# Performance work log

Measured on AMD Instinct MI355X. Metric: run time of the kernel, lower is better.

## Reference

```python
import math
import jax, jax.numpy as jnp
import numpy as np

N_HEAD = 16
HEAD_DIM = 64
TOPK = 128


def rotate_half(x):
    # interleaved rotate: (x0,x1,x2,x3,...) -> (-x1,x0,-x3,x2,...)
    x1 = x[..., ::2]
    x2 = x[..., 1::2]
    return jnp.stack((-x2, x1), axis=-1).reshape(x.shape)


def rope_tables(seq_len, head_dim):
    inv_freq = 1.0 / (10000.0 ** (jnp.arange(0, head_dim, 2, dtype=jnp.float32) / head_dim))
    t = jnp.arange(seq_len, dtype=jnp.float32)
    freqs = jnp.einsum('i,j->ij', t, inv_freq)          # [S, hd/2]
    emb = jnp.repeat(freqs, 2, axis=-1)                  # [S, hd] (repeat_interleave)
    return jnp.cos(emb)[None, None], jnp.sin(emb)[None, None]  # [1,1,S,hd]


def setup_inputs() -> dict:
    key = jax.random.key(0)
    k1, k2, k3 = jax.random.split(key, 3)
    B, S, C = 1, 2048, 1024
    x = jax.random.normal(k1, (B, S, C), dtype=jnp.float32)
    w_qkv = jax.random.normal(k2, (3 * C, C), dtype=jnp.float32) * 0.02
    w_proj = jax.random.normal(k3, (C, C), dtype=jnp.float32) * 0.02
    return {"x": x, "w_qkv": w_qkv, "w_proj": w_proj}


def reference(x, w_qkv, w_proj):
    B, S, C = x.shape
    H, hd = N_HEAD, HEAD_DIM
    neg = jnp.finfo(x.dtype).min

    qkv = x @ w_qkv.T                                   # [B,S,3C]
    q, k, v = jnp.split(qkv, 3, axis=-1)
    q = q.reshape(B, S, H, hd).transpose(0, 2, 1, 3)    # [B,H,S,hd]
    k = k.reshape(B, S, H, hd).transpose(0, 2, 1, 3)
    v = v.reshape(B, S, H, hd).transpose(0, 2, 1, 3)

    cos, sin = rope_tables(S, hd)
    q = q * cos + rotate_half(q) * sin
    k = k * cos + rotate_half(k) * sin

    # qk_norm (F.normalize, p=2, eps=1e-12)
    q = q / jnp.maximum(jnp.linalg.norm(q, axis=-1, keepdims=True), 1e-12)
    k = k / jnp.maximum(jnp.linalg.norm(k, axis=-1, keepdims=True), 1e-12)

    scores = jnp.einsum('bhqd,bhkd->bhqk', q, k) / math.sqrt(hd)  # [B,H,S,S]
    causal = jnp.tril(jnp.ones((S, S), dtype=bool))[None, None]
    scores = jnp.where(causal, scores, neg)

    # top-k sparsification (TOPK < S)
    _, idx = jax.lax.top_k(scores, TOPK)                # [B,H,S,TOPK]
    bi = jnp.arange(B)[:, None, None, None]
    hi = jnp.arange(H)[None, :, None, None]
    qi = jnp.arange(S)[None, None, :, None]
    top_mask = jnp.zeros(scores.shape, dtype=bool).at[bi, hi, qi, idx].set(True)
    top_mask = top_mask & causal
    scores = jnp.where(top_mask, scores, neg)

    att = jax.nn.softmax(scores, axis=-1)               # dropout p=0 -> identity
    y = jnp.einsum('bhqk,bhkd->bhqd', att, v)
    y = y.transpose(0, 2, 1, 3).reshape(B, S, C)
    return y @ w_proj.T
```

## Files before the change

### kernel.cpp

```cpp
#include <hip/hip_runtime.h>
#include <hip/hip_bf16.h>
#include <math.h>

#define S_LEN 2048
#define C_DIM 1024
#define NH    16
#define HD    64
#define TOPK  128

typedef __attribute__((ext_vector_type(8))) short s16x8;
typedef __attribute__((ext_vector_type(4))) float f32x4;

#define KSCALE 250000.0f
#define KINV   (1.0f / 250000.0f)
#define KOFF   0.13f
#define SUW    2056

__global__ void cvt_f32_bf16(const float* __restrict__ in, __hip_bfloat16* __restrict__ out, int n) {
    int idx = (blockIdx.x * blockDim.x + threadIdx.x) * 4;
    if (idx + 3 < n) {
        float4 v = *(const float4*)(in + idx);
        out[idx + 0] = __float2bfloat16(v.x);
        out[idx + 1] = __float2bfloat16(v.y);
        out[idx + 2] = __float2bfloat16(v.z);
        out[idx + 3] = __float2bfloat16(v.w);
    }
}

typedef const __attribute__((address_space(1))) unsigned int* gp32;
typedef __attribute__((address_space(3))) unsigned int* lp32;

__global__ __launch_bounds__(256) void gemm_bt(const __hip_bfloat16* __restrict__ A,
                                               const __hip_bfloat16* __restrict__ B,
                                               float* __restrict__ C,
                                               int M, int N, int K)
{
    __shared__ short As[128 * 32];
    __shared__ short Bs[128 * 32];
    const int bm = blockIdx.y * 128;
    const int bn = blockIdx.x * 128;
    const int tid = threadIdx.x;
    const int lane = tid & 63;
    const int wave = tid >> 6;
    const int wm = (wave >> 1) * 64;
    const int wn = (wave & 1) * 64;

    f32x4 acc[4][4] = {};

    const int srow = tid >> 2;
    const int scol = (tid & 3) * 8;
    const int fr = lane & 15;
    const int fk = (lane >> 4) * 8;

    const short* Ab = (const short*)A;
    const short* Bb = (const short*)B;

    for (int k0 = 0; k0 < K; k0 += 32) {
        __syncthreads();
        __builtin_amdgcn_global_load_lds((gp32)(Ab + (size_t)(bm + srow) * K + k0 + scol),
                                         (lp32)((char*)As + tid * 16), 16, 0, 0);
        __builtin_amdgcn_global_load_lds((gp32)(Ab + (size_t)(bm + 64 + srow) * K + k0 + scol),
                                         (lp32)((char*)As + 4096 + tid * 16), 16, 0, 0);
        __builtin_amdgcn_global_load_lds((gp32)(Bb + (size_t)(bn + srow) * K + k0 + scol),
                                         (lp32)((char*)Bs + tid * 16), 16, 0, 0);
        __builtin_amdgcn_global_load_lds((gp32)(Bb + (size_t)(bn + 64 + srow) * K + k0 + scol),
                                         (lp32)((char*)Bs + 4096 + tid * 16), 16, 0, 0);
        __syncthreads();

        s16x8 af[4], bfr[4];
        #pragma unroll
        for (int m = 0; m < 4; ++m) af[m]  = *(const s16x8*)&As[(wm + m * 16 + fr) * 32 + fk];
        #pragma unroll
        for (int n = 0; n < 4; ++n) bfr[n] = *(const s16x8*)&Bs[(wn + n * 16 + fr) * 32 + fk];
        #pragma unroll
        for (int m = 0; m < 4; ++m)
            #pragma unroll
            for (int n = 0; n < 4; ++n)
                acc[m][n] = __builtin_amdgcn_mfma_f32_16x16x32_bf16(af[m], bfr[n], acc[m][n], 0, 0, 0);
    }

    const int cr = (lane >> 4) * 4;
    const int cc = lane & 15;
    #pragma unroll
    for (int m = 0; m < 4; ++m)
        #pragma unroll
        for (int n = 0; n < 4; ++n)
            #pragma unroll
            for (int j = 0; j < 4; ++j) {
                int row = bm + wm + m * 16 + cr + j;
                int col = bn + wn + n * 16 + cc;
                C[(size_t)row * N + col] = acc[m][n][j];
            }
}

__global__ __launch_bounds__(256) void rope_norm(const float* __restrict__ qkv,
                                                 __hip_bfloat16* __restrict__ qhi,
                                                 __hip_bfloat16* __restrict__ qlo,
                                                 __hip_bfloat16* __restrict__ khi,
                                                 __hip_bfloat16* __restrict__ klo,
                                                 __hip_bfloat16* __restrict__ vh)
{
    const int gw = blockIdx.x * 4 + (threadIdx.x >> 6);
    const int lane = threadIdx.x & 63;
    const int h = gw >> 11;
    const int s = gw & 2047;
    const float* base = qkv + (size_t)s * (3 * C_DIM);
    float qx = base[h * HD + lane];
    float kx = base[C_DIM + h * HD + lane];
    float vx = base[2 * C_DIM + h * HD + lane];

    const int i = lane >> 1;
    const float invf = expf(-(float)(2 * i) * (9.210340371976184f / 64.f));
    const float ang = (float)s * invf;
    float sn, cs;
    sincosf(ang, &sn, &cs);
    float qp = __shfl_xor(qx, 1);
    float kp = __shfl_xor(kx, 1);
    const float sgn = (lane & 1) ? 1.f : -1.f;
    float qr = qx * cs + sgn * qp * sn;
    float kr = kx * cs + sgn * kp * sn;

    float s2q = qr * qr, s2k = kr * kr;
    #pragma unroll
    for (int off = 32; off > 0; off >>= 1) {
        s2q += __shfl_xor(s2q, off);
        s2k += __shfl_xor(s2k, off);
    }
    qr = qr / fmaxf(sqrtf(s2q), 1e-12f);
    kr = kr / fmaxf(sqrtf(s2k), 1e-12f);

    size_t o = ((size_t)h * S_LEN + s) * HD + lane;
    __hip_bfloat16 qh_ = __float2bfloat16(qr);
    __hip_bfloat16 kh_ = __float2bfloat16(kr);
    qhi[o] = qh_; qlo[o] = __float2bfloat16(qr - __bfloat162float(qh_));
    khi[o] = kh_; klo[o] = __float2bfloat16(kr - __bfloat162float(kh_));
    vh[o] = __float2bfloat16(vx);
}

__device__ __forceinline__ unsigned wave_prefix_incl(unsigned v, int lane) {
    #pragma unroll
    for (int off = 1; off < 64; off <<= 1) {
        unsigned t = __shfl_up(v, off);
        v += (lane >= off) ? t : 0u;
    }
    return v;
}

__device__ __forceinline__ void find_byte(const unsigned* hist256, int need, int lane,
                                          int& B, int& needRem, int& eqc)
{
    uint4 b = *(const uint4*)&hist256[lane * 4];
    unsigned sl = b.x + b.y + b.z + b.w;
    unsigned suf = sl;
    #pragma unroll
    for (int off = 1; off < 64; off <<= 1) {
        unsigned t = __shfl_down(suf, off);
        suf += (lane + off < 64) ? t : 0u;
    }
    bool qual = (suf >= (unsigned)need) && (suf - sl < (unsigned)need);
    unsigned long long mask = __ballot(qual);
    int src = (int)__builtin_ctzll(mask);

    unsigned bb0 = b.x, bb1 = b.y, bb2 = b.z, bb3 = b.w;
    unsigned cum = suf - sl;
    int myB = 0; unsigned myAbove = 0, myEq = 0;
    if (cum + bb3 >= (unsigned)need) { myB = lane * 4 + 3; myAbove = cum; myEq = bb3; }
    else {
        cum += bb3;
        if (cum + bb2 >= (unsigned)need) { myB = lane * 4 + 2; myAbove = cum; myEq = bb2; }
        else {
            cum += bb2;
            if (cum + bb1 >= (unsigned)need) { myB = lane * 4 + 1; myAbove = cum; myEq = bb1; }
            else {
                cum += bb1;
                if (cum + bb0 >= (unsigned)need) { myB = lane * 4 + 0; myAbove = cum; myEq = bb0; }
            }
        }
    }
    B = __shfl(myB, src);
    needRem = need - (int)__shfl((int)myAbove, src);
    eqc = (int)__shfl((int)myEq, src);
}

__global__ __launch_bounds__(256, 4) void attn3(const __hip_bfloat16* __restrict__ qhi,
                                                const __hip_bfloat16* __restrict__ qlo,
                                                const __hip_bfloat16* __restrict__ khi,
                                                const __hip_bfloat16* __restrict__ klo,
                                                const __hip_bfloat16* __restrict__ vhb,
                                                __hip_bfloat16* __restrict__ yb)
{
    __shared__ unsigned short su[8][SUW];
    __shared__ unsigned hist[4][256];
    __shared__ unsigned short klist[8][TOPK];

    const int q0 = blockIdx.x * 8;
    const int h = blockIdx.y;
    const int tid = threadIdx.x, lane = tid & 63, wv = tid >> 6;
    const int ntiles = (q0 + 8 + 63) >> 6;
    const int SB = ntiles * 64;
    const size_t hb = (size_t)h * S_LEN;

    const int fr = lane & 15;
    const int ak = (lane >> 4) * 8;
    const short* qp_h = (const short*)qhi + (hb + q0 + (fr & 7)) * HD;
    const short* qp_l = (const short*)qlo + (hb + q0 + (fr & 7)) * HD;
    s16x8 qa_h0 = *(const s16x8*)(qp_h + ak);
    s16x8 qa_h1 = *(const s16x8*)(qp_h + ak + 32);
    s16x8 qa_l0 = *(const s16x8*)(qp_l + ak);
    s16x8 qa_l1 = *(const s16x8*)(qp_l + ak + 32);

    for (int t = wv; t < ntiles; t += 4) {
        const int k0 = t * 64;
        #pragma unroll
        for (int cb = 0; cb < 4; ++cb) {
            const int key = k0 + cb * 16 + fr;
            const short* kh_ = (const short*)khi + (hb + key) * HD;
            const short* kl_ = (const short*)klo + (hb + key) * HD;
            s16x8 b_h0 = *(const s16x8*)(kh_ + ak);
            s16x8 b_h1 = *(const s16x8*)(kh_ + ak + 32);
            s16x8 b_l0 = *(const s16x8*)(kl_ + ak);
            s16x8 b_l1 = *(const s16x8*)(kl_ + ak + 32);
            f32x4 acc = {};
            acc = __builtin_amdgcn_mfma_f32_16x16x32_bf16(qa_h0, b_h0, acc, 0, 0, 0);
            acc = __builtin_amdgcn_mfma_f32_16x16x32_bf16(qa_h1, b_h1, acc, 0, 0, 0);
            acc = __builtin_amdgcn_mfma_f32_16x16x32_bf16(qa_h0, b_l0, acc, 0, 0, 0);
            acc = __builtin_amdgcn_mfma_f32_16x16x32_bf16(qa_h1, b_l1, acc, 0, 0, 0);
            acc = __builtin_amdgcn_mfma_f32_16x16x32_bf16(qa_l0, b_h0, acc, 0, 0, 0);
            acc = __builtin_amdgcn_mfma_f32_16x16x32_bf16(qa_l1, b_h1, acc, 0, 0, 0);
            #pragma unroll
            for (int j = 0; j < 4; ++j) {
                const int rowD = (lane >> 4) * 4 + j;
                if (rowD < 8) {
                    float s = acc[j] * 0.125f;
                    int ku = 0;
                    if (key <= q0 + rowD) {
                        ku = 1 + (int)((s + KOFF) * KSCALE);
                        ku = ku < 1 ? 1 : (ku > 65535 ? 65535 : ku);
                    }
                    su[rowD][key] = (unsigned short)ku;
                }
            }
        }
    }
    __syncthreads();

    const int nchT = (SB + 255) >> 8;

    for (int r8 = 0; r8 < 2; ++r8) {
        const int row = wv * 2 + r8;
        const int q = q0 + row;
        const int need = (q + 1 < TOPK) ? q + 1 : TOPK;

        if (q < TOPK) {
            for (int s = lane; s < need; s += 64) klist[row][s] = (unsigned short)s;
            for (int s = need + lane; s < TOPK; s += 64) klist[row][s] = 0;
        } else {
            *(uint4*)&hist[wv][lane * 4] = make_uint4(0u, 0u, 0u, 0u);
            for (int c = 0; c < nchT; ++c) {
                const int base = (c << 8) + lane * 4;
                if (base < SB) {
                    unsigned long long w8 = *(const unsigned long long*)&su[row][base];
                    unsigned k0_ = (unsigned)(w8 & 0xffff), k1_ = (unsigned)((w8 >> 16) & 0xffff);
                    unsigned k2_ = (unsigned)((w8 >> 32) & 0xffff), k3_ = (unsigned)((w8 >> 48) & 0xffff);
                    if (k0_) atomicAdd(&hist[wv][k0_ >> 8], 1u);
                    if (k1_) atomicAdd(&hist[wv][k1_ >> 8], 1u);
                    if (k2_) atomicAdd(&hist[wv][k2_ >> 8], 1u);
                    if (k3_) atomicAdd(&hist[wv][k3_ >> 8], 1u);
                }
            }
            __asm__ volatile("s_waitcnt lgkmcnt(0)" ::: "memory");
            int B1, need2, eqc1;
            find_byte(hist[wv], need, lane, B1, need2, eqc1);

            *(uint4*)&hist[wv][lane * 4] = make_uint4(0u, 0u, 0u, 0u);
            for (int c = 0; c < nchT; ++c) {
                const int base = (c << 8) + lane * 4;
                if (base < SB) {
                    unsigned long long w8 = *(const unsigned long long*)&su[row][base];
                    unsigned k0_ = (unsigned)(w8 & 0xffff), k1_ = (unsigned)((w8 >> 16) & 0xffff);
                    unsigned k2_ = (unsigned)((w8 >> 32) & 0xffff), k3_ = (unsigned)((w8 >> 48) & 0xffff);
                    if (k0_ && (k0_ >> 8) == (unsigned)B1) atomicAdd(&hist[wv][k0_ & 255u], 1u);
                    if (k1_ && (k1_ >> 8) == (unsigned)B1) atomicAdd(&hist[wv][k1_ & 255u], 1u);
                    if (k2_ && (k2_ >> 8) == (unsigned)B1) atomicAdd(&hist[wv][k2_ & 255u], 1u);
                    if (k3_ && (k3_ >> 8) == (unsigned)B1) atomicAdd(&hist[wv][k3_ & 255u], 1u);
                }
            }
            __asm__ volatile("s_waitcnt lgkmcnt(0)" ::: "memory");
            int B2, takeEq, eqc2;
            find_byte(hist[wv], need2, lane, B2, takeEq, eqc2);

            const unsigned T = ((unsigned)B1 << 8) | (unsigned)B2;
            const int gtTot = need - takeEq;
            const bool tieEasy = (takeEq == eqc2);

            int gbase = 0, te = 0;
            for (int c = 0; c < nchT; ++c) {
                const int base = (c << 8) + lane * 4;
                const bool g = base < SB;
                unsigned long long w8 = g ? *(const unsigned long long*)&su[row][base] : 0ull;
                unsigned kk[4];
                kk[0] = (unsigned)(w8 & 0xffff); kk[1] = (unsigned)((w8 >> 16) & 0xffff);
                kk[2] = (unsigned)((w8 >> 32) & 0xffff); kk[3] = (unsigned)((w8 >> 48) & 0xffff);
                bool f0, f1, f2, f3;
                if (tieEasy) { f0 = kk[0] >= T; f1 = kk[1] >= T; f2 = kk[2] >= T; f3 = kk[3] >= T; }
                else         { f0 = kk[0] >  T; f1 = kk[1] >  T; f2 = kk[2] >  T; f3 = kk[3] >  T; }
                unsigned cl = (unsigned)f0 + f1 + f2 + f3;
                unsigned inc = wave_prefix_incl(cl, lane);
                int slot = gbase + (int)(inc - cl);
                if (f0) klist[row][slot++] = (unsigned short)(base + 0);
                if (f1) klist[row][slot++] = (unsigned short)(base + 1);
                if (f2) klist[row][slot++] = (unsigned short)(base + 2);
                if (f3) klist[row][slot++] = (unsigned short)(base + 3);
                gbase += (int)__shfl((int)inc, 63);
                if (!tieEasy) {
                    #pragma unroll
                    for (int j = 0; j < 4; ++j) {
                        bool tj = g && (kk[j] == T);
                        unsigned long long bal = __ballot(tj);
                        int r = te + (int)__popcll(bal & ((1ull << lane) - 1ull));
                        if (tj && r < takeEq) klist[row][gtTot + r] = (unsigned short)(base + j);
                        te += (int)__popcll(bal);
                    }
                }
            }
        }
        __asm__ volatile("s_waitcnt lgkmcnt(0)" ::: "memory");

        const int g = lane >> 3;
        const int d0 = (lane & 7) * 8;
        const short* vb = (const short*)vhb + hb * HD;
        float acc8[8] = {0.f, 0.f, 0.f, 0.f, 0.f, 0.f, 0.f, 0.f};
        float psum = 0.f;

        #pragma unroll
        for (int half = 0; half < 2; ++half) {
            int kk[8]; float pp[8];
            #pragma unroll
            for (int b = 0; b < 8; ++b) {
                const int slot = (half * 8 + b) * 8 + g;
                const int k = klist[row][slot];
                kk[b] = k;
                pp[b] = (slot < need) ? __expf(((float)su[row][k] - 0.5f) * KINV - KOFF) : 0.f;
            }
            s16x8 vv[8];
            #pragma unroll
            for (int b = 0; b < 8; ++b) vv[b] = *(const s16x8*)(vb + (size_t)kk[b] * HD + d0);
            #pragma unroll
            for (int b = 0; b < 8; ++b) {
                psum += pp[b];
                #pragma unroll
                for (int j = 0; j < 8; ++j) {
                    unsigned short us = (unsigned short)vv[b][j];
                    float vf = __bfloat162float(*reinterpret_cast<__hip_bfloat16*>(&us));
                    acc8[j] += pp[b] * vf;
                }
            }
        }

        #pragma unroll
        for (int off = 8; off < 64; off <<= 1) {
            psum += __shfl_xor(psum, off);
            #pragma unroll
            for (int j = 0; j < 8; ++j) acc8[j] += __shfl_xor(acc8[j], off);
        }

        if (lane < 8) {
            const float inv = 1.0f / psum;
            s16x8 r;
            #pragma unroll
            for (int j = 0; j < 8; ++j) {
                __hip_bfloat16 bf = __float2bfloat16(acc8[j] * inv);
                r[j] = *reinterpret_cast<short*>(&bf);
            }
            *(s16x8*)((short*)yb + (size_t)q * C_DIM + h * HD + lane * 8) = r;
        }
    }
}

extern "C" void kernel_launch(void* const* d_in, const int* in_sizes, int n_in,
                              void* d_out, int out_size, void* d_ws, size_t ws_size,
                              hipStream_t stream)
{
    const float* x      = (const float*)d_in[0];
    const float* w_qkv  = (const float*)d_in[1];
    const float* w_proj = (const float*)d_in[2];
    float* out = (float*)d_out;

    char* ws = (char*)d_ws;
    size_t off = 0;
    auto alloc = [&](size_t bytes) -> void* {
        void* p = ws + off;
        off += (bytes + 255) & ~(size_t)255;
        return p;
    };
    __hip_bfloat16* xb  = (__hip_bfloat16*)alloc((size_t)S_LEN * C_DIM * 2);
    __hip_bfloat16* wqb = (__hip_bfloat16*)alloc((size_t)3 * C_DIM * C_DIM * 2);
    __hip_bfloat16* wpb = (__hip_bfloat16*)alloc((size_t)C_DIM * C_DIM * 2);
    float* qkvf = (float*)alloc((size_t)S_LEN * 3 * C_DIM * 4);
    __hip_bfloat16* qhi = (__hip_bfloat16*)alloc((size_t)NH * S_LEN * HD * 2);
    __hip_bfloat16* qlo = (__hip_bfloat16*)alloc((size_t)NH * S_LEN * HD * 2);
    __hip_bfloat16* khi = (__hip_bfloat16*)alloc((size_t)NH * S_LEN * HD * 2);
    __hip_bfloat16* klo = (__hip_bfloat16*)alloc((size_t)NH * S_LEN * HD * 2);
    __hip_bfloat16* vhb = (__hip_bfloat16*)alloc((size_t)NH * S_LEN * HD * 2);
    __hip_bfloat16* yb  = (__hip_bfloat16*)alloc((size_t)S_LEN * C_DIM * 2);

    int n1 = S_LEN * C_DIM, n2 = 3 * C_DIM * C_DIM, n3 = C_DIM * C_DIM;
    cvt_f32_bf16<<<n1 / 4 / 256, 256, 0, stream>>>(x, xb, n1);
    cvt_f32_bf16<<<n2 / 4 / 256, 256, 0, stream>>>(w_qkv, wqb, n2);
    cvt_f32_bf16<<<n3 / 4 / 256, 256, 0, stream>>>(w_proj, wpb, n3);

    gemm_bt<<<dim3(3 * C_DIM / 128, S_LEN / 128), 256, 0, stream>>>(xb, wqb, qkvf, S_LEN, 3 * C_DIM, C_DIM);

    rope_norm<<<NH * S_LEN / 4, 256, 0, stream>>>(qkvf, qhi, qlo, khi, klo, vhb);

    attn3<<<dim3(S_LEN / 8, NH), 256, 0, stream>>>(qhi, qlo, khi, klo, vhb, yb);

    gemm_bt<<<dim3(C_DIM / 128, S_LEN / 128), 256, 0, stream>>>(yb, wpb, out, S_LEN, C_DIM, C_DIM);
}
```

Before: 338.8 us.

## Fuse first-pass radix histogram into score write and use one wave per row

The attention kernel now runs 512 threads (8 waves) per block, so each wave owns a single query row instead of two. The first-level 256-bin histogram is built with LDS atomics while scores are written, which removes a full re-scan of the score row. Bins are packed two 16-bit counters per word, halving histogram LDS. The grid is reordered so head is the fast index, which may improve K/V cache locality, at the cost of more atomic contention during the score phase and higher occupancy pressure.

Result: slower. 405.8 us (+19.8%).

```diff
diff --git a/kernel.cpp b/kernel.cpp
--- a/kernel.cpp
+++ b/kernel.cpp
@@ -146,11 +146,10 @@
     return v;
 }
 
-__device__ __forceinline__ void find_byte(const unsigned* hist256, int need, int lane,
-                                          int& B, int& needRem, int& eqc)
+__device__ __forceinline__ void find_byte4(unsigned bb0, unsigned bb1, unsigned bb2, unsigned bb3,
+                                           int need, int lane, int& B, int& needRem, int& eqc)
 {
-    uint4 b = *(const uint4*)&hist256[lane * 4];
-    unsigned sl = b.x + b.y + b.z + b.w;
+    unsigned sl = bb0 + bb1 + bb2 + bb3;
     unsigned suf = sl;
     #pragma unroll
     for (int off = 1; off < 64; off <<= 1) {
@@ -161,7 +160,6 @@
     unsigned long long mask = __ballot(qual);
     int src = (int)__builtin_ctzll(mask);
 
-    unsigned bb0 = b.x, bb1 = b.y, bb2 = b.z, bb3 = b.w;
     unsigned cum = suf - sl;
     int myB = 0; unsigned myAbove = 0, myEq = 0;
     if (cum + bb3 >= (unsigned)need) { myB = lane * 4 + 3; myAbove = cum; myEq = bb3; }
@@ -182,7 +180,7 @@
     eqc = (int)__shfl((int)myEq, src);
 }
 
-__global__ __launch_bounds__(256, 4) void attn3(const __hip_bfloat16* __restrict__ qhi,
+__global__ __launch_bounds__(512, 8) void attn4(const __hip_bfloat16* __restrict__ qhi,
                                                 const __hip_bfloat16* __restrict__ qlo,
                                                 const __hip_bfloat16* __restrict__ khi,
                                                 const __hip_bfloat16* __restrict__ klo,
@@ -190,15 +188,18 @@
                                                 __hip_bfloat16* __restrict__ yb)
 {
     __shared__ unsigned short su[8][SUW];
-    __shared__ unsigned hist[4][256];
+    __shared__ unsigned hist[8][128];
     __shared__ unsigned short klist[8][TOPK];
 
-    const int q0 = blockIdx.x * 8;
-    const int h = blockIdx.y;
+    const int h = blockIdx.x;
+    const int q0 = blockIdx.y * 8;
     const int tid = threadIdx.x, lane = tid & 63, wv = tid >> 6;
     const int ntiles = (q0 + 8 + 63) >> 6;
     const int SB = ntiles * 64;
     const size_t hb = (size_t)h * S_LEN;
+
+    ((unsigned*)hist)[tid] = 0u;
+    ((unsigned*)hist)[tid + 512] = 0u;
 
     const int fr = lane & 15;
     const int ak = (lane >> 4) * 8;
@@ -208,8 +209,9 @@
     s16x8 qa_h1 = *(const s16x8*)(qp_h + ak + 32);
     s16x8 qa_l0 = *(const s16x8*)(qp_l + ak);
     s16x8 qa_l1 = *(const s16x8*)(qp_l + ak + 32);
-
-    for (int t = wv; t < ntiles; t += 4) {
+    __syncthreads();
+
+    for (int t = wv; t < ntiles; t += 8) {
         const int k0 = t * 64;
         #pragma unroll
         for (int cb = 0; cb < 4; ++cb) {
@@ -236,6 +238,8 @@
                     if (key <= q0 + rowD) {
                         ku = 1 + (int)((s + KOFF) * KSCALE);
                         ku = ku < 1 ? 1 : (ku > 65535 ? 65535 : ku);
+                        const int hibin = ku >> 8;
+                        atomicAdd(&hist[rowD][hibin >> 1], (hibin & 1) ? 0x10000u : 1u);
                     }
                     su[rowD][key] = (unsigned short)ku;
                 }
@@ -245,135 +249,123 @@
     __syncthreads();
 
     const int nchT = (SB + 255) >> 8;
-
-    for (int r8 = 0; r8 < 2; ++r8) {
-        const int row = wv * 2 + r8;
-        const int q = q0 + row;
-        const int need = (q + 1 < TOPK) ? q + 1 : TOPK;
-
-        if (q < TOPK) {
-            for (int s = lane; s < need; s += 64) klist[row][s] = (unsigned short)s;
-            for (int s = need + lane; s < TOPK; s += 64) klist[row][s] = 0;
-        } else {
-            *(uint4*)&hist[wv][lane * 4] = make_uint4(0u, 0u, 0u, 0u);
-            for (int c = 0; c < nchT; ++c) {
-                const int base = (c << 8) + lane * 4;
-                if (base < SB) {
-                    unsigned long long w8 = *(const unsigned long long*)&su[row][base];
-                    unsigned k0_ = (unsigned)(w8 & 0xffff), k1_ = (unsigned)((w8 >> 16) & 0xffff);
-                    unsigned k2_ = (unsigned)((w8 >> 32) & 0xffff), k3_ = (unsigned)((w8 >> 48) & 0xffff);
-                    if (k0_) atomicAdd(&hist[wv][k0_ >> 8], 1u);
-                    if (k1_) atomicAdd(&hist[wv][k1_ >> 8], 1u);
-                    if (k2_) atomicAdd(&hist[wv][k2_ >> 8], 1u);
-                    if (k3_) atomicAdd(&hist[wv][k3_ >> 8], 1u);
-                }
-            }
-            __asm__ volatile("s_waitcnt lgkmcnt(0)" ::: "memory");
-            int B1, need2, eqc1;
-            find_byte(hist[wv], need, lane, B1, need2, eqc1);
-
-            *(uint4*)&hist[wv][lane * 4] = make_uint4(0u, 0u, 0u, 0u);
-            for (int c = 0; c < nchT; ++c) {
-                const int base = (c << 8) + lane * 4;
-                if (base < SB) {
-                    unsigned long long w8 = *(const unsigned long long*)&su[row][base];
-                    unsigned k0_ = (unsigned)(w8 & 0xffff), k1_ = (unsigned)((w8 >> 16) & 0xffff);
-                    unsigned k2_ = (unsigned)((w8 >> 32) & 0xffff), k3_ = (unsigned)((w8 >> 48) & 0xffff);
-                    if (k0_ && (k0_ >> 8) == (unsigned)B1) atomicAdd(&hist[wv][k0_ & 255u], 1u);
-                    if (k1_ && (k1_ >> 8) == (unsigned)B1) atomicAdd(&hist[wv][k1_ & 255u], 1u);
-                    if (k2_ && (k2_ >> 8) == (unsigned)B1) atomicAdd(&hist[wv][k2_ & 255u], 1u);
-                    if (k3_ && (k3_ >> 8) == (unsigned)B1) atomicAdd(&hist[wv][k3_ & 255u], 1u);
-                }
-            }
-            __asm__ volatile("s_waitcnt lgkmcnt(0)" ::: "memory");
-            int B2, takeEq, eqc2;
-            find_byte(hist[wv], need2, lane, B2, takeEq, eqc2);
-
-            const unsigned T = ((unsigned)B1 << 8) | (unsigned)B2;
-            const int gtTot = need - takeEq;
-            const bool tieEasy = (takeEq == eqc2);
-
-            int gbase = 0, te = 0;
-            for (int c = 0; c < nchT; ++c) {
-                const int base = (c << 8) + lane * 4;
-                const bool g = base < SB;
-                unsigned long long w8 = g ? *(const unsigned long long*)&su[row][base] : 0ull;
-                unsigned kk[4];
-                kk[0] = (unsigned)(w8 & 0xffff); kk[1] = (unsigned)((w8 >> 16) & 0xffff);
-                kk[2] = (unsigned)((w8 >> 32) & 0xffff); kk[3] = (unsigned)((w8 >> 48) & 0xffff);
-                bool f0, f1, f2, f3;
-                if (tieEasy) { f0 = kk[0] >= T; f1 = kk[1] >= T; f2 = kk[2] >= T; f3 = kk[3] >= T; }
-                else         { f0 = kk[0] >  T; f1 = kk[1] >  T; f2 = kk[2] >  T; f3 = kk[3] >  T; }
-                unsigned cl = (unsigned)f0 + f1 + f2 + f3;
-                unsigned inc = wave_prefix_incl(cl, lane);
-                int slot = gbase + (int)(inc - cl);
-                if (f0) klist[row][slot++] = (unsigned short)(base + 0);
-                if (f1) klist[row][slot++] = (unsigned short)(base + 1);
-                if (f2) klist[row][slot++] = (unsigned short)(base + 2);
-                if (f3) klist[row][slot++] = (unsigned short)(base + 3);
-                gbase += (int)__shfl((int)inc, 63);
-                if (!tieEasy) {
-                    #pragma unroll
-                    for (int j = 0; j < 4; ++j) {
-                        bool tj = g && (kk[j] == T);
-                        unsigned long long bal = __ballot(tj);
-                        int r = te + (int)__popcll(bal & ((1ull << lane) - 1ull));
-                        if (tj && r < takeEq) klist[row][gtTot + r] = (unsigned short)(base + j);
-                        te += (int)__popcll(bal);
+    const int row = wv;
+    const int q = q0 + row;
+    const int need = (q + 1 < TOPK) ? q + 1 : TOPK;
+
+    if (q < TOPK) {
+        for (int s = lane; s < need; s += 64) klist[row][s] = (unsigned short)s;
+        for (int s = need + lane; s < TOPK; s += 64) klist[row][s] = 0;
+    } else {
+        unsigned w0 = hist[row][lane * 2], w1 = hist[row][lane * 2 + 1];
+        int B1, need2, eqc1;
+        find_byte4(w0 & 0xffffu, w0 >> 16, w1 & 0xffffu, w1 >> 16, need, lane, B1, need2, eqc1);
+
+        hist[row][lane * 2] = 0u; hist[row][lane * 2 + 1] = 0u;
+        __asm__ volatile("s_waitcnt lgkmcnt(0)" ::: "memory");
+        for (int c = 0; c < nchT; ++c) {
+            const int base = (c << 8) + lane * 4;
+            if (base < SB) {
+                unsigned long long w8 = *(const unsigned long long*)&su[row][base];
+                #pragma unroll
+                for (int jj = 0; jj < 4; ++jj) {
+                    unsigned kx = (unsigned)((w8 >> (16 * jj)) & 0xffffu);
+                    if (kx && (kx >> 8) == (unsigned)B1) {
+                        unsigned lob = kx & 255u;
+                        atomicAdd(&hist[row][lob >> 1], (lob & 1) ? 0x10000u : 1u);
                     }
                 }
             }
         }
         __asm__ volatile("s_waitcnt lgkmcnt(0)" ::: "memory");
-
-        const int g = lane >> 3;
-        const int d0 = (lane & 7) * 8;
-        const short* vb = (const short*)vhb + hb * HD;
-        float acc8[8] = {0.f, 0.f, 0.f, 0.f, 0.f, 0.f, 0.f, 0.f};
-        float psum = 0.f;
-
-        #pragma unroll
-        for (int half = 0; half < 2; ++half) {
-            int kk[8]; float pp[8];
-            #pragma unroll
-            for (int b = 0; b < 8; ++b) {
-                const int slot = (half * 8 + b) * 8 + g;
-                const int k = klist[row][slot];
-                kk[b] = k;
-                pp[b] = (slot < need) ? __expf(((float)su[row][k] - 0.5f) * KINV - KOFF) : 0.f;
-            }
-            s16x8 vv[8];
-            #pragma unroll
-            for (int b = 0; b < 8; ++b) vv[b] = *(const s16x8*)(vb + (size_t)kk[b] * HD + d0);
-            #pragma unroll
-            for (int b = 0; b < 8; ++b) {
-                psum += pp[b];
+        unsigned v0 = hist[row][lane * 2], v1 = hist[row][lane * 2 + 1];
+        int B2, takeEq, eqc2;
+        find_byte4(v0 & 0xffffu, v0 >> 16, v1 & 0xffffu, v1 >> 16, need2, lane, B2, takeEq, eqc2);
+
+        const unsigned T = ((unsigned)B1 << 8) | (unsigned)B2;
+        const int gtTot = need - takeEq;
+        const bool tieEasy = (takeEq == eqc2);
+
+        int gbase = 0, te = 0;
+        for (int c = 0; c < nchT; ++c) {
+            const int base = (c << 8) + lane * 4;
+            const bool g = base < SB;
+            unsigned long long w8 = g ? *(const unsigned long long*)&su[row][base] : 0ull;
+            unsigned kk[4];
+            kk[0] = (unsigned)(w8 & 0xffff); kk[1] = (unsigned)((w8 >> 16) & 0xffff);
+            kk[2] = (unsigned)((w8 >> 32) & 0xffff); kk[3] = (unsigned)((w8 >> 48) & 0xffff);
+            bool f0, f1, f2, f3;
+            if (tieEasy) { f0 = kk[0] >= T; f1 = kk[1] >= T; f2 = kk[2] >= T; f3 = kk[3] >= T; }
+            else         { f0 = kk[0] >  T; f1 = kk[1] >  T; f2 = kk[2] >  T; f3 = kk[3] >  T; }
+            unsigned cl = (unsigned)f0 + f1 + f2 + f3;
+            unsigned inc = wave_prefix_incl(cl, lane);
+            int slot = gbase + (int)(inc - cl);
+            if (f0) klist[row][slot++] = (unsigned short)(base + 0);
+            if (f1) klist[row][slot++] = (unsigned short)(base + 1);
+            if (f2) klist[row][slot++] = (unsigned short)(base + 2);
+            if (f3) klist[row][slot++] = (unsigned short)(base + 3);
+            gbase += (int)__shfl((int)inc, 63);
+            if (!tieEasy) {
                 #pragma unroll
-                for (int j = 0; j < 8; ++j) {
-                    unsigned short us = (unsigned short)vv[b][j];
-                    float vf = __bfloat162float(*reinterpret_cast<__hip_bfloat16*>(&us));
-                    acc8[j] += pp[b] * vf;
+                for (int j = 0; j < 4; ++j) {
+                    bool tj = g && (kk[j] == T);
+                    unsigned long long bal = __ballot(tj);
+                    int r = te + (int)__popcll(bal & ((1ull << lane) - 1ull));
+                    if (tj && r < takeEq) klist[row][gtTot + r] = (unsigned short)(base + j);
+                    te += (int)__popcll(bal);
                 }
             }
         }
-
-        #pragma unroll
-        for (int off = 8; off < 64; off <<= 1) {
-            psum += __shfl_xor(psum, off);
-            #pragma unroll
-            for (int j = 0; j < 8; ++j) acc8[j] += __shfl_xor(acc8[j], off);
-        }
-
-        if (lane < 8) {
-            const float inv = 1.0f / psum;
-            s16x8 r;
+    }
+    __asm__ volatile("s_waitcnt lgkmcnt(0)" ::: "memory");
+
+    const int g = lane >> 3;
+    const int d0 = (lane & 7) * 8;
+    const short* vb = (const short*)vhb + hb * HD;
+    float acc8[8] = {0.f, 0.f, 0.f, 0.f, 0.f, 0.f, 0.f, 0.f};
+    float psum = 0.f;
+
+    #pragma unroll
+    for (int grp = 0; grp < 4; ++grp) {
+        int kk[4]; float pp[4];
+        #pragma unroll
+        for (int b = 0; b < 4; ++b) {
+            const int slot = (grp * 4 + b) * 8 + g;
+            const int k = klist[row][slot];
+            kk[b] = k;
+            pp[b] = (slot < need) ? __expf(((float)su[row][k] - 0.5f) * KINV - KOFF) : 0.f;
+        }
+        s16x8 vv[4];
+        #pragma unroll
+        for (int b = 0; b < 4; ++b) vv[b] = *(const s16x8*)(vb + (size_t)kk[b] * HD + d0);
+        #pragma unroll
+        for (int b = 0; b < 4; ++b) {
+            psum += pp[b];
             #pragma unroll
             for (int j = 0; j < 8; ++j) {
-                __hip_bfloat16 bf = __float2bfloat16(acc8[j] * inv);
-                r[j] = *reinterpret_cast<short*>(&bf);
-            }
-            *(s16x8*)((short*)yb + (size_t)q * C_DIM + h * HD + lane * 8) = r;
-        }
+                unsigned short us = (unsigned short)vv[b][j];
+                float vf = __bfloat162float(*reinterpret_cast<__hip_bfloat16*>(&us));
+                acc8[j] += pp[b] * vf;
+            }
+        }
+    }
+
+    #pragma unroll
+    for (int off = 8; off < 64; off <<= 1) {
+        psum += __shfl_xor(psum, off);
+        #pragma unroll
+        for (int j = 0; j < 8; ++j) acc8[j] += __shfl_xor(acc8[j], off);
+    }
+
+    if (lane < 8) {
+        const float inv = 1.0f / psum;
+        s16x8 r;
+        #pragma unroll
+        for (int j = 0; j < 8; ++j) {
+            __hip_bfloat16 bf = __float2bfloat16(acc8[j] * inv);
+            r[j] = *reinterpret_cast<short*>(&bf);
+        }
+        *(s16x8*)((short*)yb + (size_t)q * C_DIM + h * HD + lane * 8) = r;
     }
 }
 
@@ -413,7 +405,7 @@
 
     rope_norm<<<NH * S_LEN / 4, 256, 0, stream>>>(qkvf, qhi, qlo, khi, klo, vhb);
 
-    attn3<<<dim3(S_LEN / 8, NH), 256, 0, stream>>>(qhi, qlo, khi, klo, vhb, yb);
+    attn4<<<dim3(NH, S_LEN / 8), 512, 0, stream>>>(qhi, qlo, khi, klo, vhb, yb);
 
     gemm_bt<<<dim3(C_DIM / 128, S_LEN / 128), 256, 0, stream>>>(yb, wpb, out, S_LEN, C_DIM, C_DIM);
 }
```
